# Optimization experiments

Measured on AMD Instinct MI355X. Metric: run time of the kernel, lower is better.

Reference implementation:

```python
import math
import jax, jax.numpy as jnp
import numpy as np

D_MODEL = 1024
NUM_SCALES = 4
STATE_SIZE = 16
EXPAND = 2
D_INNER = D_MODEL * EXPAND
D_PER_SCALE = D_INNER // NUM_SCALES
BATCH, SEQ = 4, 4096


def _make_A_log():
    base = np.arange(1, STATE_SIZE + 1, dtype=np.float32)  # (N,)
    parts = [np.broadcast_to(base * (2.0 ** i), (D_PER_SCALE, STATE_SIZE)) for i in range(NUM_SCALES)]
    A = np.concatenate(parts, axis=0)  # (d_inner, N)
    return jnp.asarray(np.log(A))


def setup_inputs() -> dict:
    key = jax.random.key(0)
    ks = jax.random.split(key, 8)
    scale = 0.02
    x = jax.random.normal(ks[0], (BATCH, SEQ, D_MODEL), dtype=jnp.float32)
    W_in = jax.random.normal(ks[1], (2 * D_INNER, D_MODEL), dtype=jnp.float32) * scale
    W_B = jax.random.normal(ks[2], (STATE_SIZE, D_INNER), dtype=jnp.float32) * scale
    W_C = jax.random.normal(ks[3], (STATE_SIZE, D_INNER), dtype=jnp.float32) * scale
    W_dt = jax.random.normal(ks[4], (D_INNER, D_INNER), dtype=jnp.float32) * scale
    # dt bias: log of dt_init ~ Uniform in log-space between 1e-3 and 1e-1
    u = jax.random.uniform(ks[5], (D_INNER,), dtype=jnp.float32)
    b_dt = u * (math.log(0.1) - math.log(0.001)) + math.log(0.001)
    W_out = jax.random.normal(ks[6], (D_MODEL, D_INNER), dtype=jnp.float32) * scale
    A_log = _make_A_log()
    D = jnp.ones((D_INNER,), dtype=jnp.float32)
    output_gate = jnp.zeros((1,), dtype=jnp.float32)
    return {"x": x, "W_in": W_in, "A_log": A_log, "W_B": W_B, "W_C": W_C,
            "W_dt": W_dt, "b_dt": b_dt, "D": D, "output_gate": output_gate, "W_out": W_out}


def _selective_scan(x_ssm, A, B_mat, C_mat, dt):
    # x_ssm: (B,L,d), A: (d,N), B_mat/C_mat: (B,L,N), dt: (B,L,d)
    b, L, d = x_ssm.shape
    N = A.shape[1]
    h0 = jnp.zeros((b, d, N), dtype=jnp.float32)

    def step(h, inp):
        dt_t, B_t, C_t, x_t = inp  # (B,d),(B,N),(B,N),(B,d)
        A_bar = jnp.exp(jnp.minimum(dt_t[..., None] * A, 20.0))       # (B,d,N)
        B_bar = dt_t[..., None] * B_t[:, None, :]                      # (B,d,N)
        h = A_bar * h + B_bar * x_t[..., None]
        y_t = jnp.einsum('bdn,bn->bd', h, C_t)
        return h, y_t

    xs = (jnp.swapaxes(dt, 0, 1), jnp.swapaxes(B_mat, 0, 1),
          jnp.swapaxes(C_mat, 0, 1), jnp.swapaxes(x_ssm, 0, 1))
    _, ys = jax.lax.scan(step, h0, xs)   # ys: (L,B,d)
    return jnp.swapaxes(ys, 0, 1)


def reference(x, W_in, A_log, W_B, W_C, W_dt, b_dt, D, output_gate, W_out):
    xz = jnp.einsum('bld,ed->ble', x, W_in)          # (B,L,2*d_inner)
    x_ssm, z = jnp.split(xz, 2, axis=-1)
    A = -jnp.exp(A_log.astype(jnp.float32))           # (d_inner,N)
    B_mat = jnp.einsum('bld,nd->bln', x_ssm, W_B)
    C_mat = jnp.einsum('bld,nd->bln', x_ssm, W_C)
    dt = jax.nn.softplus(jnp.einsum('bld,ed->ble', x_ssm, W_dt) + b_dt)
    y = _selective_scan(x_ssm.astype(jnp.float32), A,
                        B_mat.astype(jnp.float32), C_mat.astype(jnp.float32),
                        dt.astype(jnp.float32))
    y = y + x_ssm * D[None, None, :]
    y = y * jax.nn.silu(z)
    out = jnp.einsum('ble,de->bld', y, W_out) * jax.nn.sigmoid(output_gate)
    return out
```

## Files before the change

kernel.cpp:

```cpp
#include <hip/hip_runtime.h>
#include <hip/hip_bf16.h>
#include <math.h>

#define D_MODEL 1024
#define D_INNER 2048
#define NSTATE  16
#define BATCH   4
#define SEQ     4096
#define MTOT    (BATCH*SEQ)
#define SDT     2176
#define NCAT    2176
#define NCHUNK  16
#define CLEN    (SEQ/NCHUNK)
#define N1      (2*D_INNER)

typedef __attribute__((ext_vector_type(8))) __bf16 bf16x8;
typedef __attribute__((ext_vector_type(4))) float f32x4;

__device__ __forceinline__ float b2f(unsigned short u){
  return __uint_as_float(((unsigned int)u) << 16);
}
__device__ __forceinline__ unsigned short f2b(float f){
  unsigned int u = __float_as_uint(f);
  u = (u + 0x7FFFu + ((u >> 16) & 1u)) >> 16;
  return (unsigned short)u;
}
__device__ __forceinline__ float softplus_f(float x){
  float r = log1pf(__expf(-fabsf(x)));
  return x > 0.f ? x + r : r;
}

__device__ __forceinline__ void async16(unsigned short* lds, const unsigned short* g){
  __builtin_amdgcn_global_load_lds(
      (const __attribute__((address_space(1))) unsigned int*)g,
      (__attribute__((address_space(3))) unsigned int*)lds, 16, 0, 0);
}

__global__ void cvt_f2b_kernel(const float* __restrict__ src,
                               unsigned short* __restrict__ dst){
  int i = (blockIdx.x * 256 + threadIdx.x) * 4;
  float4 v = *(const float4*)(src + i);
  *(ushort2*)(dst + i)     = (ushort2){f2b(v.x), f2b(v.y)};
  *(ushort2*)(dst + i + 2) = (ushort2){f2b(v.z), f2b(v.w)};
}

__global__ void concat_w_kernel(const float* __restrict__ Wdt,
                                const float* __restrict__ WB,
                                const float* __restrict__ WC,
                                unsigned short* __restrict__ Wcat){
  int idx = blockIdx.x * 256 + threadIdx.x;
  int row = idx >> 9;
  int q   = idx & 511;
  float4 v;
  if      (row < 2048) v = *(const float4*)(Wdt + ((size_t)row * 2048 + q * 4));
  else if (row < 2064) v = *(const float4*)(WB  + ((size_t)(row - 2048) * 2048 + q * 4));
  else if (row < 2080) v = *(const float4*)(WC  + ((size_t)(row - 2064) * 2048 + q * 4));
  else                 v = make_float4(0.f, 0.f, 0.f, 0.f);
  unsigned short* p = Wcat + (size_t)idx * 4;
  *(ushort2*)(p)     = (ushort2){f2b(v.x), f2b(v.y)};
  *(ushort2*)(p + 2) = (ushort2){f2b(v.z), f2b(v.w)};
}

template<int MODE>
__global__ __launch_bounds__(256, 2) void gemm_bt(
    const unsigned short* __restrict__ A,
    const unsigned short* __restrict__ W,
    unsigned short* __restrict__ o0,
    unsigned short* __restrict__ o1,
    float* __restrict__ of,
    const float* __restrict__ bias,
    int K)
{
  const int bm = blockIdx.y, bn = blockIdx.x;
  const int tid = threadIdx.x;
  const int lane = tid & 63;
  const int w = tid >> 6;
  const int wr = w >> 1, wc = w & 1;

  __shared__ unsigned short sAd[2][128 * 64];
  __shared__ unsigned short sBd[2][128 * 64];

  f32x4 acc[4][4];
  #pragma unroll
  for (int i = 0; i < 4; i++)
    #pragma unroll
    for (int j = 0; j < 4; j++) acc[i][j] = (f32x4){0.f, 0.f, 0.f, 0.f};

  const int rw8 = lane >> 3;
  const int ch  = (lane & 7) ^ rw8;
  const unsigned short* Ag = A + (size_t)(bm * 128 + w * 32 + rw8) * K + ch * 8;
  const unsigned short* Wg = W + (size_t)(bn * 128 + w * 32 + rw8) * K + ch * 8;

  const int m16 = lane & 15, q = lane >> 4;

  #pragma unroll
  for (int it = 0; it < 4; it++)
    async16(&sAd[0][(w * 32 + it * 8) * 64], Ag + (size_t)(it * 8) * K);
  #pragma unroll
  for (int it = 0; it < 4; it++)
    async16(&sBd[0][(w * 32 + it * 8) * 64], Wg + (size_t)(it * 8) * K);

  int cur = 0;
  for (int k0 = 0; k0 < K; k0 += 64) {
    const int nxt = cur ^ 1;
    if (k0 + 64 < K) {
      #pragma unroll
      for (int it = 0; it < 4; it++)
        async16(&sAd[nxt][(w * 32 + it * 8) * 64], Ag + (size_t)(it * 8) * K + k0 + 64);
      #pragma unroll
      for (int it = 0; it < 4; it++)
        async16(&sBd[nxt][(w * 32 + it * 8) * 64], Wg + (size_t)(it * 8) * K + k0 + 64);
      asm volatile("s_waitcnt vmcnt(8)" ::: "memory");
    } else {
      asm volatile("s_waitcnt vmcnt(0)" ::: "memory");
    }
    asm volatile("s_barrier" ::: "memory");

    const unsigned short* pA = sAd[cur];
    const unsigned short* pB = sBd[cur];
    #pragma unroll
    for (int kk = 0; kk < 2; kk++) {
      bf16x8 af[4], bfr[4];
      #pragma unroll
      for (int mt = 0; mt < 4; mt++) {
        const int row = wr * 64 + mt * 16 + m16;
        af[mt] = *(const bf16x8*)&pA[row * 64 + (((kk * 4 + q) ^ (m16 & 7)) << 3)];
      }
      #pragma unroll
      for (int nt = 0; nt < 4; nt++) {
        const int row = wc * 64 + nt * 16 + m16;
        bfr[nt] = *(const bf16x8*)&pB[row * 64 + (((kk * 4 + q) ^ (m16 & 7)) << 3)];
      }
      #pragma unroll
      for (int mt = 0; mt < 4; mt++)
        #pragma unroll
        for (int nt = 0; nt < 4; nt++)
          acc[mt][nt] = __builtin_amdgcn_mfma_f32_16x16x32_bf16(
              af[mt], bfr[nt], acc[mt][nt], 0, 0, 0);
    }
    asm volatile("s_waitcnt lgkmcnt(0)" ::: "memory");
    asm volatile("s_barrier" ::: "memory");
    cur = nxt;
  }

  float gscale = 1.f;
  if (MODE == 2) gscale = 1.f / (1.f + __expf(-bias[0]));

  const int r0 = bm * 128 + wr * 64 + (q << 2);
  const int c0 = bn * 128 + wc * 64 + m16;
  #pragma unroll
  for (int mt = 0; mt < 4; mt++) {
    #pragma unroll
    for (int nt = 0; nt < 4; nt++) {
      const int col = c0 + nt * 16;
      #pragma unroll
      for (int i = 0; i < 4; i++) {
        const int row = r0 + mt * 16 + i;
        float v = acc[mt][nt][i];
        if (MODE == 0) {
          if (col < D_INNER) o0[(size_t)row * D_INNER + col] = f2b(v);
          else               o1[(size_t)row * D_INNER + (col - D_INNER)] = f2b(v);
        } else if (MODE == 1) {
          if (col < D_INNER) v = softplus_f(v + bias[col]);
          o0[(size_t)row * SDT + col] = f2b(v);
        } else {
          of[(size_t)row * D_MODEL + col] = v * gscale;
        }
      }
    }
  }
}

__global__ __launch_bounds__(256) void scan_passA(
    const unsigned short* __restrict__ dtBC,
    const unsigned short* __restrict__ xs,
    const float* __restrict__ Alog,
    float* __restrict__ Pb, float* __restrict__ Sb)
{
  const int d = blockIdx.x * 256 + threadIdx.x;
  const int b = blockIdx.y;
  const int c = blockIdx.z;

  float a[NSTATE];
  #pragma unroll
  for (int n = 0; n < NSTATE; n++) a[n] = -__expf(Alog[d * NSTATE + n]);

  float P[NSTATE], S[NSTATE];
  #pragma unroll
  for (int n = 0; n < NSTATE; n++) { P[n] = 1.f; S[n] = 0.f; }

  __shared__ float sB[16][16];
  const size_t bL = (size_t)b * SEQ;
  const int t0c = c * CLEN;
  const int lt = threadIdx.x >> 4, ln = threadIdx.x & 15;

  for (int t0 = t0c; t0 < t0c + CLEN; t0 += 16) {
    __syncthreads();
    sB[lt][ln] = b2f(dtBC[(bL + t0 + lt) * SDT + 2048 + ln]);
    __syncthreads();
    for (int tt = 0; tt < 16; tt++) {
      const size_t rw = bL + t0 + tt;
      const float dt = b2f(dtBC[rw * SDT + d]);
      const float x  = b2f(xs[rw * D_INNER + d]);
      const float dtx = dt * x;
      #pragma unroll
      for (int n = 0; n < NSTATE; n++) {
        const float ab = __expf(dt * a[n]);
        P[n] *= ab;
        S[n] = ab * S[n] + dtx * sB[tt][n];
      }
    }
  }
  const size_t base = (((size_t)c * BATCH + b) * D_INNER + d) * NSTATE;
  #pragma unroll
  for (int n = 0; n < NSTATE; n += 4) {
    *(f32x4*)&Pb[base + n] = (f32x4){P[n], P[n+1], P[n+2], P[n+3]};
    *(f32x4*)&Sb[base + n] = (f32x4){S[n], S[n+1], S[n+2], S[n+3]};
  }
}

__global__ __launch_bounds__(256) void scan_passB(float* __restrict__ Pb,
                                                  const float* __restrict__ Sb)
{
  const size_t j = (size_t)blockIdx.x * 256 + threadIdx.x;
  const size_t stride = (size_t)BATCH * D_INNER * NSTATE;
  float h = 0.f;
  for (int c = 0; c < NCHUNK; c++) {
    const size_t idx = (size_t)c * stride + j;
    const float p = Pb[idx];
    const float s = Sb[idx];
    Pb[idx] = h;
    h = p * h + s;
  }
}

__global__ __launch_bounds__(256) void scan_passC(
    const unsigned short* __restrict__ dtBC,
    const unsigned short* __restrict__ xs,
    const unsigned short* __restrict__ zb,
    const float* __restrict__ Alog,
    const float* __restrict__ Dv,
    const float* __restrict__ Hb,
    unsigned short* __restrict__ yb)
{
  const int d = blockIdx.x * 256 + threadIdx.x;
  const int b = blockIdx.y;
  const int c = blockIdx.z;

  float a[NSTATE];
  #pragma unroll
  for (int n = 0; n < NSTATE; n++) a[n] = -__expf(Alog[d * NSTATE + n]);

  float h[NSTATE];
  const size_t base = (((size_t)c * BATCH + b) * D_INNER + d) * NSTATE;
  #pragma unroll
  for (int n = 0; n < NSTATE; n += 4) {
    f32x4 v = *(const f32x4*)&Hb[base + n];
    h[n] = v.x; h[n+1] = v.y; h[n+2] = v.z; h[n+3] = v.w;
  }
  const float Dd = Dv[d];

  __shared__ float sB[16][16];
  __shared__ float sC[16][16];
  const size_t bL = (size_t)b * SEQ;
  const int t0c = c * CLEN;
  const int lt = threadIdx.x >> 4, ln = threadIdx.x & 15;

  for (int t0 = t0c; t0 < t0c + CLEN; t0 += 16) {
    __syncthreads();
    {
      const size_t rwb = (bL + t0 + lt) * SDT + 2048;
      sB[lt][ln] = b2f(dtBC[rwb + ln]);
      sC[lt][ln] = b2f(dtBC[rwb + 16 + ln]);
    }
    __syncthreads();
    for (int tt = 0; tt < 16; tt++) {
      const size_t rw = bL + t0 + tt;
      const float dt = b2f(dtBC[rw * SDT + d]);
      const float x  = b2f(xs[rw * D_INNER + d]);
      const float z  = b2f(zb[rw * D_INNER + d]);
      const float dtx = dt * x;
      float y = 0.f;
      #pragma unroll
      for (int n = 0; n < NSTATE; n++) {
        const float ab = __expf(dt * a[n]);
        h[n] = ab * h[n] + dtx * sB[tt][n];
        y += h[n] * sC[tt][n];
      }
      y = (y + x * Dd) * (z / (1.f + __expf(-z)));
      yb[rw * D_INNER + d] = f2b(y);
    }
  }
}

extern "C" void kernel_launch(void* const* d_in, const int* in_sizes, int n_in,
                              void* d_out, int out_size, void* d_ws, size_t ws_size,
                              hipStream_t stream)
{
  const float* x    = (const float*)d_in[0];
  const float* Win  = (const float*)d_in[1];
  const float* Alog = (const float*)d_in[2];
  const float* WB   = (const float*)d_in[3];
  const float* WC   = (const float*)d_in[4];
  const float* Wdt  = (const float*)d_in[5];
  const float* bdt  = (const float*)d_in[6];
  const float* Dv   = (const float*)d_in[7];
  const float* gate = (const float*)d_in[8];
  const float* Wout = (const float*)d_in[9];
  float* outp = (float*)d_out;

  char* ws = (char*)d_ws;
  unsigned short* xs    = (unsigned short*)(ws + 0);
  unsigned short* zy    = (unsigned short*)(ws + 67108864);
  unsigned short* dtBC  = (unsigned short*)(ws + 134217728);
  unsigned short* Winb  = (unsigned short*)(ws + 205520896);
  unsigned short* Woutb = (unsigned short*)(ws + 213909504);

  char* ob = (char*)d_out;
  float* Pb = (float*)(ob + 0);
  float* Sb = (float*)(ob + 8388608);
  unsigned short* Wcatb = (unsigned short*)(ob + 16777216);
  unsigned short* xb    = (unsigned short*)(ob + 33554432);

  cvt_f2b_kernel<<<16384, 256, 0, stream>>>(x, xb);
  cvt_f2b_kernel<<<4096, 256, 0, stream>>>(Win, Winb);
  cvt_f2b_kernel<<<2048, 256, 0, stream>>>(Wout, Woutb);
  concat_w_kernel<<<4352, 256, 0, stream>>>(Wdt, WB, WC, Wcatb);

  gemm_bt<0><<<dim3(N1 / 128, MTOT / 128), 256, 0, stream>>>(
      xb, Winb, xs, zy, nullptr, nullptr, D_MODEL);
  gemm_bt<1><<<dim3(NCAT / 128, MTOT / 128), 256, 0, stream>>>(
      xs, Wcatb, dtBC, nullptr, nullptr, bdt, D_INNER);
  scan_passA<<<dim3(D_INNER / 256, BATCH, NCHUNK), 256, 0, stream>>>(
      dtBC, xs, Alog, Pb, Sb);
  scan_passB<<<(BATCH * D_INNER * NSTATE) / 256, 256, 0, stream>>>(Pb, Sb);
  scan_passC<<<dim3(D_INNER / 256, BATCH, NCHUNK), 256, 0, stream>>>(
      dtBC, xs, zy, Alog, Dv, Pb, zy);
  gemm_bt<2><<<dim3(D_MODEL / 128, MTOT / 128), 256, 0, stream>>>(
      zy, Woutb, nullptr, nullptr, outp, gate, D_INNER);
}
```

Measured before the change: 1.116 ms.

## Rewrite bf16 GEMM as 256x256 tile, 8-wave kernel with interleaved staging

The shared GEMM kernel goes from a 128x128 tile with 4 waves to a 256x256 tile with 8 waves. K is handled as 128-wide double-buffered stages, where LDS loads, async global loads and MFMA quarters are interleaved under s_setprio and barriers. Workgroup indices are remapped in a stride-8 swizzle to improve L2 locality. The concatenated dt/B/C weight is padded to 2304 columns to fit the larger tile, and stores past SDT are masked. This raises per-block data reuse and overlaps memory traffic with compute, at the cost of more registers and LDS (64KB per block) and wasted work on the padded columns.

```diff
diff --git a/kernel.cpp b/kernel.cpp
--- a/kernel.cpp
+++ b/kernel.cpp
@@ -9,7 +9,7 @@
 #define SEQ     4096
 #define MTOT    (BATCH*SEQ)
 #define SDT     2176
-#define NCAT    2176
+#define NCATP   2304
 #define NCHUNK  16
 #define CLEN    (SEQ/NCHUNK)
 #define N1      (2*D_INNER)
@@ -62,7 +62,7 @@
 }
 
 template<int MODE>
-__global__ __launch_bounds__(256, 2) void gemm_bt(
+__global__ __launch_bounds__(512, 2) void gemm_bt(
     const unsigned short* __restrict__ A,
     const unsigned short* __restrict__ W,
     unsigned short* __restrict__ o0,
@@ -71,85 +71,132 @@
     const float* __restrict__ bias,
     int K)
 {
-  const int bm = blockIdx.y, bn = blockIdx.x;
-  const int tid = threadIdx.x;
+  const int tid  = threadIdx.x;
   const int lane = tid & 63;
-  const int w = tid >> 6;
-  const int wr = w >> 1, wc = w & 1;
-
-  __shared__ unsigned short sAd[2][128 * 64];
-  __shared__ unsigned short sBd[2][128 * 64];
-
-  f32x4 acc[4][4];
-  #pragma unroll
-  for (int i = 0; i < 4; i++)
+  const int w    = tid >> 6;
+  const int wm   = w >> 2;
+  const int wn   = w & 3;
+  const int m16  = lane & 15, q = lane >> 4;
+
+  const int gx  = gridDim.x;
+  const int nwg = gx * gridDim.y;
+  int flat = blockIdx.y * gx + blockIdx.x;
+  flat = (flat & 7) * (nwg >> 3) + (flat >> 3);
+  const int bm = flat / gx;
+  const int bn = flat - bm * gx;
+
+  __shared__ unsigned short sA[2][16384];
+  __shared__ unsigned short sB[2][16384];
+
+  f32x4 acc[8][4];
+  #pragma unroll
+  for (int i = 0; i < 8; i++)
     #pragma unroll
     for (int j = 0; j < 4; j++) acc[i][j] = (f32x4){0.f, 0.f, 0.f, 0.f};
 
-  const int rw8 = lane >> 3;
-  const int ch  = (lane & 7) ^ rw8;
-  const unsigned short* Ag = A + (size_t)(bm * 128 + w * 32 + rw8) * K + ch * 8;
-  const unsigned short* Wg = W + (size_t)(bn * 128 + w * 32 + rw8) * K + ch * 8;
-
-  const int m16 = lane & 15, q = lane >> 4;
-
-  #pragma unroll
-  for (int it = 0; it < 4; it++)
-    async16(&sAd[0][(w * 32 + it * 8) * 64], Ag + (size_t)(it * 8) * K);
-  #pragma unroll
-  for (int it = 0; it < 4; it++)
-    async16(&sBd[0][(w * 32 + it * 8) * 64], Wg + (size_t)(it * 8) * K);
-
-  int cur = 0;
-  for (int k0 = 0; k0 < K; k0 += 64) {
-    const int nxt = cur ^ 1;
-    if (k0 + 64 < K) {
-      #pragma unroll
-      for (int it = 0; it < 4; it++)
-        async16(&sAd[nxt][(w * 32 + it * 8) * 64], Ag + (size_t)(it * 8) * K + k0 + 64);
-      #pragma unroll
-      for (int it = 0; it < 4; it++)
-        async16(&sBd[nxt][(w * 32 + it * 8) * 64], Wg + (size_t)(it * 8) * K + k0 + 64);
-      asm volatile("s_waitcnt vmcnt(8)" ::: "memory");
-    } else {
-      asm volatile("s_waitcnt vmcnt(0)" ::: "memory");
-    }
-    asm volatile("s_barrier" ::: "memory");
-
-    const unsigned short* pA = sAd[cur];
-    const unsigned short* pB = sBd[cur];
-    #pragma unroll
-    for (int kk = 0; kk < 2; kk++) {
-      bf16x8 af[4], bfr[4];
-      #pragma unroll
-      for (int mt = 0; mt < 4; mt++) {
-        const int row = wr * 64 + mt * 16 + m16;
-        af[mt] = *(const bf16x8*)&pA[row * 64 + (((kk * 4 + q) ^ (m16 & 7)) << 3)];
-      }
-      #pragma unroll
-      for (int nt = 0; nt < 4; nt++) {
-        const int row = wc * 64 + nt * 16 + m16;
-        bfr[nt] = *(const bf16x8*)&pB[row * 64 + (((kk * 4 + q) ^ (m16 & 7)) << 3)];
-      }
-      #pragma unroll
-      for (int mt = 0; mt < 4; mt++)
-        #pragma unroll
-        for (int nt = 0; nt < 4; nt++)
-          acc[mt][nt] = __builtin_amdgcn_mfma_f32_16x16x32_bf16(
-              af[mt], bfr[nt], acc[mt][nt], 0, 0, 0);
-    }
-    asm volatile("s_waitcnt lgkmcnt(0)" ::: "memory");
-    asm volatile("s_barrier" ::: "memory");
-    cur = nxt;
-  }
+  const int ch = (tid & 7) ^ ((tid >> 3) & 7);
+  const unsigned short* Ag = A + (size_t)(bm * 256 + (tid >> 3)) * K + ch * 8;
+  const unsigned short* Wg = W + (size_t)(bn * 256 + (tid >> 3)) * K + ch * 8;
+
+#define STAGE_A(buf, h, t) do { \
+    async16(&sA[buf][(h)*8192 + w*512],        Ag + (size_t)((h)*128)*K      + (t)*64); \
+    async16(&sA[buf][(h)*8192 + 4096 + w*512], Ag + (size_t)((h)*128 + 64)*K + (t)*64); \
+  } while(0)
+#define STAGE_B(buf, h, t) do { \
+    async16(&sB[buf][(h)*8192 + w*512],        Wg + (size_t)((h)*128)*K      + (t)*64); \
+    async16(&sB[buf][(h)*8192 + 4096 + w*512], Wg + (size_t)((h)*128 + 64)*K + (t)*64); \
+  } while(0)
+
+#define LDA(dst, buf, mh) do { \
+    _Pragma("unroll") for (int mt = 0; mt < 4; mt++) \
+    _Pragma("unroll") for (int kk = 0; kk < 2; kk++) { \
+      const int row_ = wm*128 + (mh)*64 + mt*16 + m16; \
+      dst[mt][kk] = *(const bf16x8*)&sA[buf][row_*64 + (((kk*4 + q) ^ (m16 & 7)) << 3)]; \
+    } } while(0)
+#define LDB(dst, buf, nh) do { \
+    _Pragma("unroll") for (int nt = 0; nt < 2; nt++) \
+    _Pragma("unroll") for (int kk = 0; kk < 2; kk++) { \
+      const int row_ = wn*64 + (nh)*32 + nt*16 + m16; \
+      dst[nt][kk] = *(const bf16x8*)&sB[buf][row_*64 + (((kk*4 + q) ^ (m16 & 7)) << 3)]; \
+    } } while(0)
+
+#define MMAQ(Aa, Bb, MH, NH) do { \
+    __builtin_amdgcn_s_setprio(1); \
+    _Pragma("unroll") for (int kk = 0; kk < 2; kk++) \
+    _Pragma("unroll") for (int mt = 0; mt < 4; mt++) \
+    _Pragma("unroll") for (int nt = 0; nt < 2; nt++) \
+      acc[(MH)*4 + mt][(NH)*2 + nt] = __builtin_amdgcn_mfma_f32_16x16x32_bf16( \
+          Aa[mt][kk], Bb[nt][kk], acc[(MH)*4 + mt][(NH)*2 + nt], 0, 0, 0); \
+    __builtin_amdgcn_s_setprio(0); \
+    __builtin_amdgcn_sched_barrier(0); \
+  } while(0)
+
+#define BAR()  asm volatile("s_barrier" ::: "memory")
+#define LGK0() do { asm volatile("s_waitcnt lgkmcnt(0)" ::: "memory"); \
+                    __builtin_amdgcn_sched_barrier(0); } while(0)
+
+  STAGE_A(0, 0, 0); STAGE_A(0, 1, 0); STAGE_B(0, 0, 0); STAGE_B(0, 1, 0);
+  STAGE_A(1, 0, 1); STAGE_A(1, 1, 1);
+  asm volatile("s_waitcnt vmcnt(4)" ::: "memory");
+  BAR();
+
+  auto run_iter = [&](int t0, bool last) {
+    bf16x8 a[4][2], a2[4][2], bb0[2][2], bb1[2][2];
+    LDA(a, 0, 0); LDB(bb0, 0, 0);
+    STAGE_B(1, 0, t0 + 1);
+    BAR(); LGK0();
+    MMAQ(a, bb0, 0, 0);
+    BAR();
+    LDA(a2, 0, 1);
+    STAGE_B(1, 1, t0 + 1);
+    BAR(); LGK0();
+    MMAQ(a2, bb0, 1, 0);
+    BAR();
+    LDB(bb1, 0, 1);
+    if (!last) STAGE_A(0, 0, t0 + 2);
+    BAR(); LGK0();
+    MMAQ(a, bb1, 0, 1);
+    BAR();
+    if (!last) STAGE_A(0, 1, t0 + 2);
+    BAR();
+    MMAQ(a2, bb1, 1, 1);
+    if (last) asm volatile("s_waitcnt vmcnt(0)" ::: "memory");
+    else      asm volatile("s_waitcnt vmcnt(4)" ::: "memory");
+    BAR();
+    LDA(a, 1, 0); LDB(bb0, 1, 0);
+    if (!last) STAGE_B(0, 0, t0 + 2);
+    BAR(); LGK0();
+    MMAQ(a, bb0, 0, 0);
+    BAR();
+    LDA(a2, 1, 1);
+    if (!last) STAGE_B(0, 1, t0 + 2);
+    BAR(); LGK0();
+    MMAQ(a2, bb0, 1, 0);
+    BAR();
+    LDB(bb1, 1, 1);
+    if (!last) STAGE_A(1, 0, t0 + 3);
+    BAR(); LGK0();
+    MMAQ(a, bb1, 0, 1);
+    BAR();
+    if (!last) STAGE_A(1, 1, t0 + 3);
+    BAR();
+    MMAQ(a2, bb1, 1, 1);
+    if (!last) asm volatile("s_waitcnt vmcnt(4)" ::: "memory");
+    BAR();
+  };
+
+  const int NIT = K >> 7;
+  #pragma unroll 1
+  for (int j = 0; j < NIT - 1; j++) run_iter(2 * j, false);
+  run_iter(2 * (NIT - 1), true);
 
   float gscale = 1.f;
   if (MODE == 2) gscale = 1.f / (1.f + __expf(-bias[0]));
 
-  const int r0 = bm * 128 + wr * 64 + (q << 2);
-  const int c0 = bn * 128 + wc * 64 + m16;
-  #pragma unroll
-  for (int mt = 0; mt < 4; mt++) {
+  const int r0 = bm * 256 + wm * 128 + (q << 2);
+  const int c0 = bn * 256 + wn * 64 + m16;
+  #pragma unroll
+  for (int mt = 0; mt < 8; mt++) {
     #pragma unroll
     for (int nt = 0; nt < 4; nt++) {
       const int col = c0 + nt * 16;
@@ -162,13 +209,20 @@
           else               o1[(size_t)row * D_INNER + (col - D_INNER)] = f2b(v);
         } else if (MODE == 1) {
           if (col < D_INNER) v = softplus_f(v + bias[col]);
-          o0[(size_t)row * SDT + col] = f2b(v);
+          if (col < SDT)     o0[(size_t)row * SDT + col] = f2b(v);
         } else {
           of[(size_t)row * D_MODEL + col] = v * gscale;
         }
       }
     }
   }
+#undef STAGE_A
+#undef STAGE_B
+#undef LDA
+#undef LDB
+#undef MMAQ
+#undef BAR
+#undef LGK0
 }
 
 __global__ __launch_bounds__(256) void scan_passA(
@@ -325,17 +379,17 @@
   cvt_f2b_kernel<<<16384, 256, 0, stream>>>(x, xb);
   cvt_f2b_kernel<<<4096, 256, 0, stream>>>(Win, Winb);
   cvt_f2b_kernel<<<2048, 256, 0, stream>>>(Wout, Woutb);
-  concat_w_kernel<<<4352, 256, 0, stream>>>(Wdt, WB, WC, Wcatb);
-
-  gemm_bt<0><<<dim3(N1 / 128, MTOT / 128), 256, 0, stream>>>(
+  concat_w_kernel<<<(NCATP * D_INNER / 4) / 256, 256, 0, stream>>>(Wdt, WB, WC, Wcatb);
+
+  gemm_bt<0><<<dim3(N1 / 256, MTOT / 256), 512, 0, stream>>>(
       xb, Winb, xs, zy, nullptr, nullptr, D_MODEL);
-  gemm_bt<1><<<dim3(NCAT / 128, MTOT / 128), 256, 0, stream>>>(
+  gemm_bt<1><<<dim3(NCATP / 256, MTOT / 256), 512, 0, stream>>>(
       xs, Wcatb, dtBC, nullptr, nullptr, bdt, D_INNER);
   scan_passA<<<dim3(D_INNER / 256, BATCH, NCHUNK), 256, 0, stream>>>(
       dtBC, xs, Alog, Pb, Sb);
   scan_passB<<<(BATCH * D_INNER * NSTATE) / 256, 256, 0, stream>>>(Pb, Sb);
   scan_passC<<<dim3(D_INNER / 256, BATCH, NCHUNK), 256, 0, stream>>>(
       dtBC, xs, zy, Alog, Dv, Pb, zy);
-  gemm_bt<2><<<dim3(D_MODEL / 128, MTOT / 128), 256, 0, stream>>>(
+  gemm_bt<2><<<dim3(D_MODEL / 256, MTOT / 256), 512, 0, stream>>>(
       zy, Woutb, nullptr, nullptr, outp, gate, D_INNER);
 }
```

Measured after the change: 1.350 ms. 1.21x slower.
